# Optimization experiments

Hardware: AMD Instinct MI355X
Metric: run time of the kernel (lower is better)

The kernel has to match this reference:

```python
import jax, jax.numpy as jnp
import numpy as np

N_EP = 32          # episodes; 2*N_EP total sets (Dtrain + Dtest)
S = 1024           # points per set
IN_DIM = 255       # input feature dim
T_DIM = 1          # target dim
D = IN_DIM + T_DIM # attention-1 input dim = 256
L = 512            # latent_space_dim
K = 10             # n_discrete_states


def setup_inputs() -> dict:
    key = jax.random.key(0)
    ks = jax.random.split(key, 18)
    g = lambda k, sh, sc: (jax.random.normal(k, sh, dtype=jnp.float32) * sc)
    d = {
        "x_sets": g(ks[0], (2 * N_EP, S, IN_DIM), 1.0),
        "y_sets": g(ks[1], (2 * N_EP, S, T_DIM), 1.0),
        # self-attention layer 1 (D -> L), no pooling
        "Wq1": g(ks[2], (D, L), 1.0 / np.sqrt(D)), "bq1": jnp.zeros((L,), jnp.float32),
        "Wk1": g(ks[3], (D, L), 1.0 / np.sqrt(D)), "bk1": jnp.zeros((L,), jnp.float32),
        "Wv1": g(ks[4], (D, L), 1.0 / np.sqrt(D)), "bv1": jnp.zeros((L,), jnp.float32),
        # self-attention layer 2 (L -> L), mean pooling over set dim
        "Wq2": g(ks[5], (L, L), 1.0 / np.sqrt(L)), "bq2": jnp.zeros((L,), jnp.float32),
        "Wk2": g(ks[6], (L, L), 1.0 / np.sqrt(L)), "bk2": jnp.zeros((L,), jnp.float32),
        "Wv2": g(ks[7], (L, L), 1.0 / np.sqrt(L)), "bv2": jnp.zeros((L,), jnp.float32),
        # logit encoder Linear(L, L*K)
        "We": g(ks[8], (L, L * K), 1.0 / np.sqrt(L)),
        "be": jnp.zeros((L * K,), jnp.float32),
    }
    return d


def self_attention(x, Wq, bq, Wk, bk, Wv, bv, pool_mean):
    # x: [B, S, Din]; standard scaled dot-product self-attention
    q = x @ Wq + bq                                   # [B,S,L]
    k = x @ Wk + bk                                   # [B,S,L]
    v = x @ Wv + bv                                   # [B,S,L]
    scores = jnp.einsum('bqd,bkd->bqk', q, k) / jnp.sqrt(jnp.asarray(q.shape[-1], q.dtype))
    attn = jax.nn.softmax(scores, axis=-1)            # [B,S,S]
    out = jnp.einsum('bqk,bkd->bqd', attn, v)         # [B,S,L]
    if pool_mean:
        out = out.mean(axis=1)                        # [B,L]
    return out


def reference(x_sets, y_sets,
              Wq1, bq1, Wk1, bk1, Wv1, bv1,
              Wq2, bq2, Wk2, bk2, Wv2, bv2,
              We, be):
    # DatasetFeatureExtractor: cat(features, targets) -> attn -> relu -> attn(pool) -> relu
    x = jnp.concatenate([x_sets, y_sets], axis=-1)    # [2n,S,D]
    h = jax.nn.relu(self_attention(x, Wq1, bq1, Wk1, bk1, Wv1, bv1, pool_mean=False))
    phi = jax.nn.relu(self_attention(h, Wq2, bq2, Wk2, bk2, Wv2, bv2, pool_mean=True))  # [2n,L]
    # logit encode + log_softmax over discrete states
    logits = (phi @ We + be).reshape(-1, L, K)        # [2n,L,K]
    logp = jax.nn.log_softmax(logits, axis=2)
    log_probs_a, log_probs_b = logp[:N_EP], logp[N_EP:]
    return log_probs_a, log_probs_b
```

## Files before the change

kernel.cpp:

```cpp
#include <hip/hip_runtime.h>
#include <hip/hip_bf16.h>
#include <math.h>

#define NB      64
#define S_LEN   1024
#define IN_DIM  255
#define D_IN    256
#define L_DIM   512
#define K_CLS   10
#define QL_ELEMS (65536L * 512)

#define TILE 64
#define BKK  16

typedef __hip_bfloat16 bf16;
typedef __attribute__((ext_vector_type(8))) short short8;
typedef __attribute__((ext_vector_type(4))) float f32x4;

__device__ __forceinline__ float u2f(unsigned short u) {
    return __uint_as_float(((unsigned int)u) << 16);
}
__device__ __forceinline__ unsigned short f2bu(float x) {
    bf16 b = __float2bfloat16(x);
    return *reinterpret_cast<unsigned short*>(&b);
}

typedef const __attribute__((address_space(1))) unsigned int* gas_t;
typedef __attribute__((address_space(3))) unsigned int* las_t;
__device__ __forceinline__ void gload16(const bf16* g, bf16* l) {
    __builtin_amdgcn_global_load_lds((gas_t)(const void*)g, (las_t)(void*)l, 16, 0, 0);
}

__global__ __launch_bounds__(256) void build_xb(const float* __restrict__ xs,
                                                const float* __restrict__ ys,
                                                bf16* __restrict__ X) {
    long i = (long)blockIdx.x * 256 + threadIdx.x;
    long m = i >> 8;
    int  kk = (int)(i & 255);
    float v = (kk < IN_DIM) ? xs[m * IN_DIM + kk] : ys[m];
    X[i] = __float2bfloat16(v);
}

struct TW {
    const float* s0; const float* s1; const float* s2; const float* s3; const float* s4;
    bf16* d0; bf16* d1; bf16* d2; bf16* d3; bf16* d4;
    const float* bq1; const float* bk1; const float* bv1;
    const float* bq2; const float* bk2;
    float* biasQKV;
    float* bias2;
};
__global__ __launch_bounds__(256) void transpose_all(TW tw) {
    int i = blockIdx.x * 256 + threadIdx.x;
    if (i < 917504) {
        const float* S; bf16* D; int K, j;
        if (i < 131072)      { S = tw.s0; D = tw.d0; K = 256; j = i; }
        else if (i < 262144) { S = tw.s1; D = tw.d1; K = 256; j = i - 131072; }
        else if (i < 393216) { S = tw.s2; D = tw.d2; K = 256; j = i - 262144; }
        else if (i < 655360) { S = tw.s3; D = tw.d3; K = 512; j = i - 393216; }
        else                 { S = tw.s4; D = tw.d4; K = 512; j = i - 655360; }
        int n = j / K, k = j - n * K;
        D[j] = __float2bfloat16(S[(long)k * 512 + n]);
    } else if (i < 919040) {
        int j = i - 917504;
        float v = (j < 512) ? tw.bq1[j] : (j < 1024 ? tw.bk1[j - 512] : tw.bv1[j - 1024]);
        tw.biasQKV[j] = v;
    } else if (i < 920064) {
        int j = i - 919040;
        tw.bias2[j] = (j < 512) ? tw.bq2[j] : tw.bk2[j - 512];
    }
}

template <bool TRANSC, bool RELU, bool HASBIAS, bool EXPO, bool RSCALE, bool WRITEC, int FUSE, bool WCOL>
__global__ __launch_bounds__(256) void gemm_mfma(const bf16* __restrict__ A,
                                                 const bf16* __restrict__ B,
                                                 const float* __restrict__ bias,
                                                 bf16* __restrict__ C,
                                                 int K, long sA, long sB, long sC,
                                                 int ldc, float alpha,
                                                 float* __restrict__ ps,
                                                 const float* __restrict__ rsinv) {
    __shared__ bf16 As[2][128 * 32];
    __shared__ bf16 Bs[2][128 * 32];

    const int gx = gridDim.x, gy = gridDim.y;
    const int nwg = gx * gy * gridDim.z;
    int orig = blockIdx.x + gx * (blockIdx.y + gy * blockIdx.z);
    int id = ((nwg & 7) == 0) ? ((orig & 7) * (nwg >> 3) + (orig >> 3)) : orig;
    const int bx = id % gx;
    const int byz = id / gx;
    const int by = byz % gy;
    const int bz = byz / gy;

    A += (long)bz * sA;
    B += (long)bz * sB;
    C += (long)bz * sC;
    const int bm = by * 128;
    const int bn = bx * 128;
    const int t  = threadIdx.x;
    const int ln = t & 63;
    const int wv = t >> 6;
    const int wm = wv >> 1;
    const int wn = wv & 1;

    const bf16* gA = A + (long)(bm + (t >> 2)) * K + (t & 3) * 8;
    const bf16* gB = B + (long)(bn + (t >> 2)) * K + (t & 3) * 8;
    const int wb = wv * 512;

    f32x4 acc[4][4];
    #pragma unroll
    for (int i = 0; i < 4; ++i)
        #pragma unroll
        for (int j = 0; j < 4; ++j)
            #pragma unroll
            for (int q = 0; q < 4; ++q) acc[i][j][q] = 0.f;

    const int ro = ln & 15;
    const int ko = (ln >> 4) * 8;

    auto stage = [&](int buf, int k0) {
        gload16(gA + k0,          As[buf] + wb);
        gload16(gA + 64 * K + k0, As[buf] + wb + 2048);
        gload16(gB + k0,          Bs[buf] + wb);
        gload16(gB + 64 * K + k0, Bs[buf] + wb + 2048);
    };

    const int nt = K >> 5;
    stage(0, 0);
    __syncthreads();

    for (int tt = 0; tt < nt; ++tt) {
        const int cur = tt & 1;
        if (tt + 1 < nt) stage(cur ^ 1, (tt + 1) << 5);

        short8 af[4], bg[4];
        #pragma unroll
        for (int i = 0; i < 4; ++i) {
            af[i] = *(const short8*)(As[cur] + (wm * 64 + i * 16 + ro) * 32 + ko);
            bg[i] = *(const short8*)(Bs[cur] + (wn * 64 + i * 16 + ro) * 32 + ko);
        }
        #pragma unroll
        for (int i = 0; i < 4; ++i)
            #pragma unroll
            for (int j = 0; j < 4; ++j)
                acc[i][j] = __builtin_amdgcn_mfma_f32_16x16x32_bf16(af[i], bg[j], acc[i][j], 0, 0, 0);
        __syncthreads();
    }

    const int r0 = bm + wm * 64 + (ln >> 4) * 4;
    const int c0 = bn + wn * 64 + (ln & 15);

    if constexpr (FUSE > 0) {
        const int seg = bn >> 9;
        if (FUSE == 1 && seg == 2) {
            bf16* Cs = C + 2 * QL_ELEMS;
            #pragma unroll
            for (int i = 0; i < 4; ++i) {
                const int rowb = r0 + i * 16;
                #pragma unroll
                for (int j = 0; j < 4; ++j) {
                    const int col = c0 + j * 16;
                    const float bi = bias[col];
                    ushort4 o;
                    o.x = f2bu(acc[i][j][0] + bi);
                    o.y = f2bu(acc[i][j][1] + bi);
                    o.z = f2bu(acc[i][j][2] + bi);
                    o.w = f2bu(acc[i][j][3] + bi);
                    *(ushort4*)(Cs + (long)(col - 1024) * 1024 + rowb) = o;
                }
            }
        } else {
            bf16* Cs = C + (long)seg * QL_ELEMS;
            #pragma unroll
            for (int i = 0; i < 4; ++i) {
                #pragma unroll
                for (int j = 0; j < 4; ++j) {
                    const int col = c0 + j * 16;
                    const float bi = bias[col];
                    const int cl = col - seg * 512;
                    #pragma unroll
                    for (int q = 0; q < 4; ++q)
                        Cs[(long)(r0 + i * 16 + q) * 512 + cl] = __float2bfloat16(acc[i][j][q] + bi);
                }
            }
        }
    } else if constexpr (TRANSC) {
        #pragma unroll
        for (int i = 0; i < 4; ++i) {
            const int rowb = r0 + i * 16;
            #pragma unroll
            for (int j = 0; j < 4; ++j) {
                const int col = c0 + j * 16;
                const float bi = HASBIAS ? bias[col] : 0.f;
                ushort4 o;
                float v0 = acc[i][j][0] * alpha + bi;
                float v1 = acc[i][j][1] * alpha + bi;
                float v2 = acc[i][j][2] * alpha + bi;
                float v3 = acc[i][j][3] * alpha + bi;
                if (RELU) { v0 = fmaxf(v0, 0.f); v1 = fmaxf(v1, 0.f); v2 = fmaxf(v2, 0.f); v3 = fmaxf(v3, 0.f); }
                o.x = f2bu(v0); o.y = f2bu(v1); o.z = f2bu(v2); o.w = f2bu(v3);
                *(ushort4*)(C + (long)col * ldc + rowb) = o;
            }
        }
    } else if constexpr (EXPO) {
        float sloc[4][4];
        #pragma unroll
        for (int i = 0; i < 4; ++i)
            #pragma unroll
            for (int q = 0; q < 4; ++q) sloc[i][q] = 0.f;
        #pragma unroll
        for (int i = 0; i < 4; ++i) {
            #pragma unroll
            for (int j = 0; j < 4; ++j) {
                const int col = c0 + j * 16;
                #pragma unroll
                for (int q = 0; q < 4; ++q) {
                    float e = __expf(fminf(acc[i][j][q] * alpha, 80.f));
                    sloc[i][q] += e;
                    if (WRITEC) C[(long)(r0 + i * 16 + q) * ldc + col] = __float2bfloat16(e);
                }
            }
        }
        #pragma unroll
        for (int o = 1; o < 16; o <<= 1)
            #pragma unroll
            for (int i = 0; i < 4; ++i)
                #pragma unroll
                for (int q = 0; q < 4; ++q)
                    sloc[i][q] += __shfl_xor(sloc[i][q], o, 64);
        if ((ln & 15) == 0) {
            const int cb = bx * 2 + wn;
            const int rb = bm + wm * 64 + (ln >> 4) * 4;
            #pragma unroll
            for (int i = 0; i < 4; ++i)
                #pragma unroll
                for (int q = 0; q < 4; ++q)
                    ps[((long)bz * 16 + cb) * 1024 + rb + i * 16 + q] = sloc[i][q];
        }
    } else if constexpr (WCOL) {
        float rsv[4][4];
        const int rb = bm + wm * 64 + (ln >> 4) * 4;
        #pragma unroll
        for (int i = 0; i < 4; ++i)
            #pragma unroll
            for (int q = 0; q < 4; ++q)
                rsv[i][q] = rsinv[(long)bz * 1024 + rb + i * 16 + q];
        float cs[4];
        #pragma unroll
        for (int j = 0; j < 4; ++j) cs[j] = 0.f;
        #pragma unroll
        for (int i = 0; i < 4; ++i)
            #pragma unroll
            for (int j = 0; j < 4; ++j)
                #pragma unroll
                for (int q = 0; q < 4; ++q)
                    cs[j] += __expf(fminf(acc[i][j][q] * alpha, 80.f)) * rsv[i][q];
        #pragma unroll
        for (int j = 0; j < 4; ++j) {
            cs[j] += __shfl_xor(cs[j], 16, 64);
            cs[j] += __shfl_xor(cs[j], 32, 64);
        }
        if (ln < 16) {
            const int cb = by * 2 + wm;
            #pragma unroll
            for (int j = 0; j < 4; ++j)
                ps[((long)bz * 16 + cb) * 1024 + (bn + wn * 64 + j * 16 + ln)] = cs[j];
        }
    } else {
        float rsv[4][4];
        if constexpr (RSCALE) {
            const int rb = bm + wm * 64 + (ln >> 4) * 4;
            #pragma unroll
            for (int i = 0; i < 4; ++i)
                #pragma unroll
                for (int q = 0; q < 4; ++q)
                    rsv[i][q] = rsinv[(long)bz * 1024 + rb + i * 16 + q];
        }
        #pragma unroll
        for (int i = 0; i < 4; ++i) {
            #pragma unroll
            for (int j = 0; j < 4; ++j) {
                const int col = c0 + j * 16;
                const float bi = HASBIAS ? bias[col] : 0.f;
                #pragma unroll
                for (int q = 0; q < 4; ++q) {
                    float v = acc[i][j][q] * alpha + bi;
                    if (RSCALE) v *= rsv[i][q];
                    if (RELU) v = fmaxf(v, 0.f);
                    C[(long)(r0 + i * 16 + q) * ldc + col] = __float2bfloat16(v);
                }
            }
        }
    }
}

__global__ __launch_bounds__(256) void rowsum_inv(const float* __restrict__ ps,
                                                  float* __restrict__ rsinv, int n) {
    int i = blockIdx.x * 256 + threadIdx.x;
    if (i >= n) return;
    const int b = i >> 10, row = i & 1023;
    float s = 0.f;
    #pragma unroll
    for (int cb = 0; cb < 16; ++cb) s += ps[((long)b * 16 + cb) * 1024 + row];
    rsinv[i] = 1.f / s;
}

__global__ __launch_bounds__(256) void colsum_red(const float* __restrict__ wps,
                                                  float* __restrict__ w, int n) {
    int i = blockIdx.x * 256 + threadIdx.x;
    if (i >= n) return;
    const int b = i >> 10, col = i & 1023;
    float s = 0.f;
    #pragma unroll
    for (int cb = 0; cb < 16; ++cb) s += wps[((long)b * 16 + cb) * 1024 + col];
    w[i] = s;
}

template <bool RELU>
__global__ __launch_bounds__(256) void gemm_f32s(const float* __restrict__ A,
                                                 const float* __restrict__ B,
                                                 const float* __restrict__ bias,
                                                 float* __restrict__ C,
                                                 int M, int N, int K) {
    __shared__ float As[BKK][TILE + 1];
    __shared__ float Bs[BKK][TILE + 1];
    const int bm = blockIdx.y * TILE;
    const int bn = blockIdx.x * TILE;
    const int t  = threadIdx.x;
    const int tx = t & 15, ty = t >> 4;
    float acc[4][4] = {};
    for (int k0 = 0; k0 < K; k0 += BKK) {
        {
            int m  = t >> 2;
            int kq = (t & 3) * 4;
            const float4 av = *(const float4*)(A + (long)(bm + m) * K + k0 + kq);
            As[kq + 0][m] = av.x; As[kq + 1][m] = av.y;
            As[kq + 2][m] = av.z; As[kq + 3][m] = av.w;
        }
        {
            int k  = t >> 4;
            int nq = (t & 15) * 4;
            const float4 bv = *(const float4*)(B + (long)(k0 + k) * N + bn + nq);
            Bs[k][nq + 0] = bv.x; Bs[k][nq + 1] = bv.y;
            Bs[k][nq + 2] = bv.z; Bs[k][nq + 3] = bv.w;
        }
        __syncthreads();
        #pragma unroll
        for (int k = 0; k < BKK; ++k) {
            float a[4], bb[4];
            #pragma unroll
            for (int i = 0; i < 4; ++i) a[i] = As[k][ty * 4 + i];
            #pragma unroll
            for (int j = 0; j < 4; ++j) bb[j] = Bs[k][tx * 4 + j];
            #pragma unroll
            for (int i = 0; i < 4; ++i)
                #pragma unroll
                for (int j = 0; j < 4; ++j)
                    acc[i][j] = fmaf(a[i], bb[j], acc[i][j]);
        }
        __syncthreads();
    }
    #pragma unroll
    for (int i = 0; i < 4; ++i) {
        const int row  = bm + ty * 4 + i;
        const int col0 = bn + tx * 4;
        #pragma unroll
        for (int j = 0; j < 4; ++j) {
            float x = acc[i][j] + bias[col0 + j];
            if (RELU) x = fmaxf(x, 0.f);
            C[(long)row * N + col0 + j] = x;
        }
    }
}

__global__ __launch_bounds__(256) void pool_u_part(const bf16* __restrict__ h,
                                                   const float* __restrict__ w,
                                                   float* __restrict__ up) {
    const int b  = blockIdx.x;
    const int qq = blockIdx.y;
    const int t  = threadIdx.x;
    __shared__ float wl[256];
    wl[t] = w[b * S_LEN + qq * 256 + t];
    __syncthreads();
    const bf16* hp = h + (long)b * S_LEN * L_DIM + (long)qq * 256 * L_DIM;
    float a0 = 0.f, a1 = 0.f;
    for (int q = 0; q < 256; ++q) {
        ushort2 uv = *(const ushort2*)(hp + (long)q * L_DIM + t * 2);
        float ww = wl[q];
        a0 = fmaf(ww, u2f(uv.x), a0);
        a1 = fmaf(ww, u2f(uv.y), a1);
    }
    up[((long)(b * 4 + qq)) * L_DIM + t * 2 + 0] = a0;
    up[((long)(b * 4 + qq)) * L_DIM + t * 2 + 1] = a1;
}

__global__ __launch_bounds__(256) void pool_u_red(const float* __restrict__ up,
                                                  float* __restrict__ u) {
    int i = blockIdx.x * 256 + threadIdx.x;
    if (i >= NB * L_DIM) return;
    int b = i >> 9, d = i & 511;
    float s = up[((long)(b * 4 + 0)) * L_DIM + d] + up[((long)(b * 4 + 1)) * L_DIM + d]
            + up[((long)(b * 4 + 2)) * L_DIM + d] + up[((long)(b * 4 + 3)) * L_DIM + d];
    u[i] = s * (1.f / (float)S_LEN);
}

__global__ __launch_bounds__(256) void log_softmax10(const float* __restrict__ logits,
                                                     float* __restrict__ out) {
    const int t = blockIdx.x * 256 + threadIdx.x;
    if (t >= NB * L_DIM) return;
    const float* p = logits + (long)t * K_CLS;
    float v[K_CLS], m = -INFINITY;
    #pragma unroll
    for (int k = 0; k < K_CLS; ++k) { v[k] = p[k]; m = fmaxf(m, v[k]); }
    float s = 0.f;
    #pragma unroll
    for (int k = 0; k < K_CLS; ++k) s += __expf(v[k] - m);
    const float lse = m + logf(s);
    float* o = out + (long)t * K_CLS;
    #pragma unroll
    for (int k = 0; k < K_CLS; ++k) o[k] = v[k] - lse;
}

extern "C" void kernel_launch(void* const* d_in, const int* in_sizes, int n_in,
                              void* d_out, int out_size, void* d_ws, size_t ws_size,
                              hipStream_t stream) {
    const float* xs  = (const float*)d_in[0];
    const float* ys  = (const float*)d_in[1];
    const float* Wq1 = (const float*)d_in[2];  const float* bq1 = (const float*)d_in[3];
    const float* Wk1 = (const float*)d_in[4];  const float* bk1 = (const float*)d_in[5];
    const float* Wv1 = (const float*)d_in[6];  const float* bv1 = (const float*)d_in[7];
    const float* Wq2 = (const float*)d_in[8];  const float* bq2 = (const float*)d_in[9];
    const float* Wk2 = (const float*)d_in[10]; const float* bk2 = (const float*)d_in[11];
    const float* Wv2 = (const float*)d_in[12]; const float* bv2 = (const float*)d_in[13];
    const float* We  = (const float*)d_in[14]; const float* be  = (const float*)d_in[15];
    float* out = (float*)d_out;

    const long M  = (long)NB * S_LEN;
    const long QL = M * L_DIM;
    const long SL = (long)S_LEN * L_DIM;
    const long SS = (long)S_LEN * S_LEN;

    bf16* Xb  = (bf16*)d_ws;
    bf16* B1  = Xb + M * D_IN;
    bf16* B2  = B1 + QL;
    bf16* B3  = B2 + QL;
    bf16* WTb = B3 + QL;
    bf16* Wq1T = WTb;
    bf16* Wk1T = Wq1T + L_DIM * D_IN;
    bf16* Wv1T = Wk1T + L_DIM * D_IN;
    bf16* Wq2T = Wv1T + L_DIM * D_IN;
    bf16* Wk2T = Wq2T + L_DIM * L_DIM;
    bf16* Scb  = Wk2T + L_DIM * L_DIM;

    const size_t base_b = (size_t)((char*)Scb - (char*)d_ws);
    const size_t f32_b  = (size_t)(M + 2 * NB * L_DIM + NB * L_DIM * K_CLS
                                   + 64 * 16 * 1024 + 64 * 1024 + 4 * NB * L_DIM
                                   + 64 * 16 * 1024 + 1536 + 1024) * 4 + 256;
    int BCH1 = 16;
    while (BCH1 > 8 && base_b + (size_t)BCH1 * SS * 2 + f32_b > ws_size) BCH1 >>= 1;

    float* w       = (float*)(Scb + (long)BCH1 * SS);
    float* u       = w   + M / S_LEN * 1024;
    float* phi     = u   + NB * L_DIM;
    float* lg      = phi + NB * L_DIM;
    float* ps      = lg  + NB * L_DIM * K_CLS;
    float* rsinv   = ps  + 64 * 16 * 1024;
    float* up      = rsinv + 64 * 1024;
    float* wps     = up  + 4 * NB * L_DIM;
    float* biasQKV = wps + 64 * 16 * 1024;
    float* bias2   = biasQKV + 1536;

    const float inv_sqrt_L = 0.044194173824159216f;

    build_xb<<<dim3((unsigned)(M * D_IN / 256)), 256, 0, stream>>>(xs, ys, Xb);
    {
        TW tw { Wq1, Wk1, Wv1, Wq2, Wk2, Wq1T, Wk1T, Wv1T, Wq2T, Wk2T,
                bq1, bk1, bv1, bq2, bk2, biasQKV, bias2 };
        transpose_all<<<dim3(3595), 256, 0, stream>>>(tw);
    }

    {
        dim3 g(1536 / 128, S_LEN / 128, NB);
        gemm_mfma<false, false, true, false, false, true, 1, false><<<g, 256, 0, stream>>>(
            Xb, WTb, biasQKV, B1, D_IN, (long)S_LEN * D_IN, 0, SL, L_DIM, 1.f, nullptr, nullptr);
    }
    for (int c = 0; c < NB / BCH1; ++c) {
        const long aoff = (long)c * BCH1 * SL;
        float* psc = ps    + (long)c * BCH1 * 16 * 1024;
        float* rsc = rsinv + (long)c * BCH1 * 1024;
        dim3 gs(S_LEN / 128, S_LEN / 128, BCH1);
        gemm_mfma<false, false, false, true, false, true, 0, false><<<gs, 256, 0, stream>>>(
            B1 + aoff, B2 + aoff, nullptr, Scb, L_DIM, SL, SL, SS, S_LEN, inv_sqrt_L, psc, nullptr);
        rowsum_inv<<<dim3((unsigned)(BCH1 * S_LEN / 256)), 256, 0, stream>>>(psc, rsc, BCH1 * S_LEN);
        dim3 gp(L_DIM / 128, S_LEN / 128, BCH1);
        gemm_mfma<false, true, false, false, true, true, 0, false><<<gp, 256, 0, stream>>>(
            Scb, B3 + aoff, nullptr, B1 + aoff, S_LEN, SS, SL, SL, L_DIM, 1.f, nullptr, rsc);
    }
    {
        dim3 g(1024 / 128, S_LEN / 128, NB);
        gemm_mfma<false, false, true, false, false, true, 2, false><<<g, 256, 0, stream>>>(
            B1, Wq2T, bias2, B2, L_DIM, SL, 0, SL, L_DIM, 1.f, nullptr, nullptr);
    }
    {
        dim3 gs(S_LEN / 128, S_LEN / 128, NB);
        gemm_mfma<false, false, false, true, false, false, 0, false><<<gs, 256, 0, stream>>>(
            B2, B3, nullptr, Scb, L_DIM, SL, SL, 0, S_LEN, inv_sqrt_L, ps, nullptr);
        rowsum_inv<<<dim3((unsigned)(NB * S_LEN / 256)), 256, 0, stream>>>(ps, rsinv, NB * S_LEN);
        gemm_mfma<false, false, false, false, false, false, 0, true><<<gs, 256, 0, stream>>>(
            B2, B3, nullptr, Scb, L_DIM, SL, SL, 0, S_LEN, inv_sqrt_L, wps, rsinv);
        colsum_red<<<dim3((unsigned)(NB * S_LEN / 256)), 256, 0, stream>>>(wps, w, NB * S_LEN);
    }
    pool_u_part<<<dim3(NB, 4), 256, 0, stream>>>(B1, w, up);
    pool_u_red<<<dim3(NB * L_DIM / 256), 256, 0, stream>>>(up, u);
    gemm_f32s<true><<<dim3(L_DIM / TILE, 1), 256, 0, stream>>>(u, Wv2, bv2, phi, NB, L_DIM, L_DIM);
    gemm_f32s<false><<<dim3((L_DIM * K_CLS) / TILE, 1), 256, 0, stream>>>(phi, We, be, lg, NB, L_DIM * K_CLS, L_DIM);
    log_softmax10<<<dim3((NB * L_DIM + 255) / 256), 256, 0, stream>>>(lg, out);
}
```

Baseline: 831.9 us.

## Fold small reduction kernels into neighbouring GEMMs and merge prep launches

Merges build_xb into the weight-transpose prep kernel. The row-sum inverse is now computed inside the consuming GEMMs, which read the partial sums into shared memory. The column-sum reduction moves into pool_u_part, and the pool reduction plus mean scaling moves into the phi GEMM's A-tile load. This removes five small kernel launches and their intermediate buffers, and drops the unused TRANSC template path. In exchange, each GEMM block redundantly sums 16 partials per row, and pool blocks re-sum the column partials.

```diff
diff --git a/kernel.cpp b/kernel.cpp
--- a/kernel.cpp
+++ b/kernel.cpp
@@ -31,17 +31,8 @@
     __builtin_amdgcn_global_load_lds((gas_t)(const void*)g, (las_t)(void*)l, 16, 0, 0);
 }
 
-__global__ __launch_bounds__(256) void build_xb(const float* __restrict__ xs,
-                                                const float* __restrict__ ys,
-                                                bf16* __restrict__ X) {
-    long i = (long)blockIdx.x * 256 + threadIdx.x;
-    long m = i >> 8;
-    int  kk = (int)(i & 255);
-    float v = (kk < IN_DIM) ? xs[m * IN_DIM + kk] : ys[m];
-    X[i] = __float2bfloat16(v);
-}
-
 struct TW {
+    const float* xs; const float* ys; bf16* X;
     const float* s0; const float* s1; const float* s2; const float* s3; const float* s4;
     bf16* d0; bf16* d1; bf16* d2; bf16* d3; bf16* d4;
     const float* bq1; const float* bk1; const float* bv1;
@@ -49,28 +40,37 @@
     float* biasQKV;
     float* bias2;
 };
-__global__ __launch_bounds__(256) void transpose_all(TW tw) {
-    int i = blockIdx.x * 256 + threadIdx.x;
-    if (i < 917504) {
+#define X_ELEMS 16777216L
+__global__ __launch_bounds__(256) void prep_all(TW tw) {
+    long i = (long)blockIdx.x * 256 + threadIdx.x;
+    if (i < X_ELEMS) {
+        long m = i >> 8;
+        int  kk = (int)(i & 255);
+        float v = (kk < IN_DIM) ? tw.xs[m * IN_DIM + kk] : tw.ys[m];
+        tw.X[i] = __float2bfloat16(v);
+        return;
+    }
+    int j0 = (int)(i - X_ELEMS);
+    if (j0 < 917504) {
         const float* S; bf16* D; int K, j;
-        if (i < 131072)      { S = tw.s0; D = tw.d0; K = 256; j = i; }
-        else if (i < 262144) { S = tw.s1; D = tw.d1; K = 256; j = i - 131072; }
-        else if (i < 393216) { S = tw.s2; D = tw.d2; K = 256; j = i - 262144; }
-        else if (i < 655360) { S = tw.s3; D = tw.d3; K = 512; j = i - 393216; }
-        else                 { S = tw.s4; D = tw.d4; K = 512; j = i - 655360; }
+        if (j0 < 131072)      { S = tw.s0; D = tw.d0; K = 256; j = j0; }
+        else if (j0 < 262144) { S = tw.s1; D = tw.d1; K = 256; j = j0 - 131072; }
+        else if (j0 < 393216) { S = tw.s2; D = tw.d2; K = 256; j = j0 - 262144; }
+        else if (j0 < 655360) { S = tw.s3; D = tw.d3; K = 512; j = j0 - 393216; }
+        else                  { S = tw.s4; D = tw.d4; K = 512; j = j0 - 655360; }
         int n = j / K, k = j - n * K;
         D[j] = __float2bfloat16(S[(long)k * 512 + n]);
-    } else if (i < 919040) {
-        int j = i - 917504;
+    } else if (j0 < 919040) {
+        int j = j0 - 917504;
         float v = (j < 512) ? tw.bq1[j] : (j < 1024 ? tw.bk1[j - 512] : tw.bv1[j - 1024]);
         tw.biasQKV[j] = v;
-    } else if (i < 920064) {
-        int j = i - 919040;
+    } else if (j0 < 920064) {
+        int j = j0 - 919040;
         tw.bias2[j] = (j < 512) ? tw.bq2[j] : tw.bk2[j - 512];
     }
 }
 
-template <bool TRANSC, bool RELU, bool HASBIAS, bool EXPO, bool RSCALE, bool WRITEC, int FUSE, bool WCOL>
+template <bool RELU, bool HASBIAS, bool EXPO, bool RSCALE, bool WRITEC, int FUSE, bool WCOL>
 __global__ __launch_bounds__(256) void gemm_mfma(const bf16* __restrict__ A,
                                                  const bf16* __restrict__ B,
                                                  const float* __restrict__ bias,
@@ -78,9 +78,10 @@
                                                  int K, long sA, long sB, long sC,
                                                  int ldc, float alpha,
                                                  float* __restrict__ ps,
-                                                 const float* __restrict__ rsinv) {
+                                                 const float* __restrict__ psIn) {
     __shared__ bf16 As[2][128 * 32];
     __shared__ bf16 Bs[2][128 * 32];
+    __shared__ float rsl[128];
 
     const int gx = gridDim.x, gy = gridDim.y;
     const int nwg = gx * gy * gridDim.z;
@@ -105,6 +106,16 @@
     const bf16* gA = A + (long)(bm + (t >> 2)) * K + (t & 3) * 8;
     const bf16* gB = B + (long)(bn + (t >> 2)) * K + (t & 3) * 8;
     const int wb = wv * 512;
+
+    if constexpr (RSCALE || WCOL) {
+        if (t < 128) {
+            float s = 0.f;
+            #pragma unroll
+            for (int cb = 0; cb < 16; ++cb)
+                s += psIn[((long)bz * 16 + cb) * 1024 + bm + t];
+            rsl[t] = 1.f / s;
+        }
+    }
 
     f32x4 acc[4][4];
     #pragma unroll
@@ -183,24 +194,6 @@
                 }
             }
         }
-    } else if constexpr (TRANSC) {
-        #pragma unroll
-        for (int i = 0; i < 4; ++i) {
-            const int rowb = r0 + i * 16;
-            #pragma unroll
-            for (int j = 0; j < 4; ++j) {
-                const int col = c0 + j * 16;
-                const float bi = HASBIAS ? bias[col] : 0.f;
-                ushort4 o;
-                float v0 = acc[i][j][0] * alpha + bi;
-                float v1 = acc[i][j][1] * alpha + bi;
-                float v2 = acc[i][j][2] * alpha + bi;
-                float v3 = acc[i][j][3] * alpha + bi;
-                if (RELU) { v0 = fmaxf(v0, 0.f); v1 = fmaxf(v1, 0.f); v2 = fmaxf(v2, 0.f); v3 = fmaxf(v3, 0.f); }
-                o.x = f2bu(v0); o.y = f2bu(v1); o.z = f2bu(v2); o.w = f2bu(v3);
-                *(ushort4*)(C + (long)col * ldc + rowb) = o;
-            }
-        }
     } else if constexpr (EXPO) {
         float sloc[4][4];
         #pragma unroll
@@ -238,12 +231,12 @@
         }
     } else if constexpr (WCOL) {
         float rsv[4][4];
-        const int rb = bm + wm * 64 + (ln >> 4) * 4;
+        const int lr = wm * 64 + (ln >> 4) * 4;
         #pragma unroll
         for (int i = 0; i < 4; ++i)
             #pragma unroll
             for (int q = 0; q < 4; ++q)
-                rsv[i][q] = rsinv[(long)bz * 1024 + rb + i * 16 + q];
+                rsv[i][q] = rsl[lr + i * 16 + q];
         float cs[4];
         #pragma unroll
         for (int j = 0; j < 4; ++j) cs[j] = 0.f;
@@ -268,12 +261,12 @@
     } else {
         float rsv[4][4];
         if constexpr (RSCALE) {
-            const int rb = bm + wm * 64 + (ln >> 4) * 4;
+            const int lr = wm * 64 + (ln >> 4) * 4;
             #pragma unroll
             for (int i = 0; i < 4; ++i)
                 #pragma unroll
                 for (int q = 0; q < 4; ++q)
-                    rsv[i][q] = rsinv[(long)bz * 1024 + rb + i * 16 + q];
+                    rsv[i][q] = rsl[lr + i * 16 + q];
         }
         #pragma unroll
         for (int i = 0; i < 4; ++i) {
@@ -293,29 +286,93 @@
     }
 }
 
-__global__ __launch_bounds__(256) void rowsum_inv(const float* __restrict__ ps,
-                                                  float* __restrict__ rsinv, int n) {
-    int i = blockIdx.x * 256 + threadIdx.x;
-    if (i >= n) return;
-    const int b = i >> 10, row = i & 1023;
-    float s = 0.f;
+__global__ __launch_bounds__(256) void pool_u_part(const bf16* __restrict__ h,
+                                                   const float* __restrict__ wps,
+                                                   float* __restrict__ up) {
+    const int b  = blockIdx.x;
+    const int qq = blockIdx.y;
+    const int t  = threadIdx.x;
+    __shared__ float wl[256];
+    {
+        float s = 0.f;
+        #pragma unroll
+        for (int cb = 0; cb < 16; ++cb)
+            s += wps[((long)b * 16 + cb) * 1024 + qq * 256 + t];
+        wl[t] = s;
+    }
+    __syncthreads();
+    const bf16* hp = h + (long)b * S_LEN * L_DIM + (long)qq * 256 * L_DIM;
+    float a0 = 0.f, a1 = 0.f;
+    for (int q = 0; q < 256; ++q) {
+        ushort2 uv = *(const ushort2*)(hp + (long)q * L_DIM + t * 2);
+        float ww = wl[q];
+        a0 = fmaf(ww, u2f(uv.x), a0);
+        a1 = fmaf(ww, u2f(uv.y), a1);
+    }
+    up[((long)(b * 4 + qq)) * L_DIM + t * 2 + 0] = a0;
+    up[((long)(b * 4 + qq)) * L_DIM + t * 2 + 1] = a1;
+}
+
+__global__ __launch_bounds__(256) void gemm_phi(const float* __restrict__ up,
+                                                const float* __restrict__ B,
+                                                const float* __restrict__ bias,
+                                                float* __restrict__ C) {
+    __shared__ float As[BKK][TILE + 1];
+    __shared__ float Bs[BKK][TILE + 1];
+    const int bn = blockIdx.x * TILE;
+    const int t  = threadIdx.x;
+    const int tx = t & 15, ty = t >> 4;
+    float acc[4][4] = {};
+    for (int k0 = 0; k0 < L_DIM; k0 += BKK) {
+        {
+            int m  = t >> 2;
+            int kq = (t & 3) * 4;
+            const float* pb = up + (long)m * 4 * L_DIM + k0 + kq;
+            float4 p0 = *(const float4*)(pb);
+            float4 p1 = *(const float4*)(pb + L_DIM);
+            float4 p2 = *(const float4*)(pb + 2 * L_DIM);
+            float4 p3 = *(const float4*)(pb + 3 * L_DIM);
+            const float sc = 1.f / (float)S_LEN;
+            As[kq + 0][m] = (p0.x + p1.x + p2.x + p3.x) * sc;
+            As[kq + 1][m] = (p0.y + p1.y + p2.y + p3.y) * sc;
+            As[kq + 2][m] = (p0.z + p1.z + p2.z + p3.z) * sc;
+            As[kq + 3][m] = (p0.w + p1.w + p2.w + p3.w) * sc;
+        }
+        {
+            int k  = t >> 4;
+            int nq = (t & 15) * 4;
+            const float4 bv = *(const float4*)(B + (long)(k0 + k) * L_DIM + bn + nq);
+            Bs[k][nq + 0] = bv.x; Bs[k][nq + 1] = bv.y;
+            Bs[k][nq + 2] = bv.z; Bs[k][nq + 3] = bv.w;
+        }
+        __syncthreads();
+        #pragma unroll
+        for (int k = 0; k < BKK; ++k) {
+            float a[4], bb[4];
+            #pragma unroll
+            for (int i = 0; i < 4; ++i) a[i] = As[k][ty * 4 + i];
+            #pragma unroll
+            for (int j = 0; j < 4; ++j) bb[j] = Bs[k][tx * 4 + j];
+            #pragma unroll
+            for (int i = 0; i < 4; ++i)
+                #pragma unroll
+                for (int j = 0; j < 4; ++j)
+                    acc[i][j] = fmaf(a[i], bb[j], acc[i][j]);
+        }
+        __syncthreads();
+    }
     #pragma unroll
-    for (int cb = 0; cb < 16; ++cb) s += ps[((long)b * 16 + cb) * 1024 + row];
-    rsinv[i] = 1.f / s;
-}
-
-__global__ __launch_bounds__(256) void colsum_red(const float* __restrict__ wps,
-                                                  float* __restrict__ w, int n) {
-    int i = blockIdx.x * 256 + threadIdx.x;
-    if (i >= n) return;
-    const int b = i >> 10, col = i & 1023;
-    float s = 0.f;
-    #pragma unroll
-    for (int cb = 0; cb < 16; ++cb) s += wps[((long)b * 16 + cb) * 1024 + col];
-    w[i] = s;
-}
-
-template <bool RELU>
+    for (int i = 0; i < 4; ++i) {
+        const int row  = ty * 4 + i;
+        const int col0 = bn + tx * 4;
+        #pragma unroll
+        for (int j = 0; j < 4; ++j) {
+            float x = fmaxf(acc[i][j] + bias[col0 + j], 0.f);
+            C[(long)row * L_DIM + col0 + j] = x;
+        }
+    }
+}
+
 __global__ __launch_bounds__(256) void gemm_f32s(const float* __restrict__ A,
                                                  const float* __restrict__ B,
                                                  const float* __restrict__ bias,
@@ -365,42 +422,9 @@
         const int col0 = bn + tx * 4;
         #pragma unroll
         for (int j = 0; j < 4; ++j) {
-            float x = acc[i][j] + bias[col0 + j];
-            if (RELU) x = fmaxf(x, 0.f);
-            C[(long)row * N + col0 + j] = x;
-        }
-    }
-}
-
-__global__ __launch_bounds__(256) void pool_u_part(const bf16* __restrict__ h,
-                                                   const float* __restrict__ w,
-                                                   float* __restrict__ up) {
-    const int b  = blockIdx.x;
-    const int qq = blockIdx.y;
-    const int t  = threadIdx.x;
-    __shared__ float wl[256];
-    wl[t] = w[b * S_LEN + qq * 256 + t];
-    __syncthreads();
-    const bf16* hp = h + (long)b * S_LEN * L_DIM + (long)qq * 256 * L_DIM;
-    float a0 = 0.f, a1 = 0.f;
-    for (int q = 0; q < 256; ++q) {
-        ushort2 uv = *(const ushort2*)(hp + (long)q * L_DIM + t * 2);
-        float ww = wl[q];
-        a0 = fmaf(ww, u2f(uv.x), a0);
-        a1 = fmaf(ww, u2f(uv.y), a1);
-    }
-    up[((long)(b * 4 + qq)) * L_DIM + t * 2 + 0] = a0;
-    up[((long)(b * 4 + qq)) * L_DIM + t * 2 + 1] = a1;
-}
-
-__global__ __launch_bounds__(256) void pool_u_red(const float* __restrict__ up,
-                                                  float* __restrict__ u) {
-    int i = blockIdx.x * 256 + threadIdx.x;
-    if (i >= NB * L_DIM) return;
-    int b = i >> 9, d = i & 511;
-    float s = up[((long)(b * 4 + 0)) * L_DIM + d] + up[((long)(b * 4 + 1)) * L_DIM + d]
-            + up[((long)(b * 4 + 2)) * L_DIM + d] + up[((long)(b * 4 + 3)) * L_DIM + d];
-    u[i] = s * (1.f / (float)S_LEN);
+            C[(long)row * N + col0 + j] = acc[i][j] + bias[col0 + j];
+        }
+    }
 }
 
 __global__ __launch_bounds__(256) void log_softmax10(const float* __restrict__ logits,
@@ -452,66 +476,57 @@
     bf16* Scb  = Wk2T + L_DIM * L_DIM;
 
     const size_t base_b = (size_t)((char*)Scb - (char*)d_ws);
-    const size_t f32_b  = (size_t)(M + 2 * NB * L_DIM + NB * L_DIM * K_CLS
-                                   + 64 * 16 * 1024 + 64 * 1024 + 4 * NB * L_DIM
+    const size_t f32_b  = (size_t)(NB * L_DIM + NB * L_DIM * K_CLS
+                                   + 64 * 16 * 1024 + 4 * NB * L_DIM
                                    + 64 * 16 * 1024 + 1536 + 1024) * 4 + 256;
     int BCH1 = 16;
     while (BCH1 > 8 && base_b + (size_t)BCH1 * SS * 2 + f32_b > ws_size) BCH1 >>= 1;
 
-    float* w       = (float*)(Scb + (long)BCH1 * SS);
-    float* u       = w   + M / S_LEN * 1024;
-    float* phi     = u   + NB * L_DIM;
+    float* phi     = (float*)(Scb + (long)BCH1 * SS);
     float* lg      = phi + NB * L_DIM;
     float* ps      = lg  + NB * L_DIM * K_CLS;
-    float* rsinv   = ps  + 64 * 16 * 1024;
-    float* up      = rsinv + 64 * 1024;
+    float* up      = ps  + 64 * 16 * 1024;
     float* wps     = up  + 4 * NB * L_DIM;
     float* biasQKV = wps + 64 * 16 * 1024;
     float* bias2   = biasQKV + 1536;
 
     const float inv_sqrt_L = 0.044194173824159216f;
 
-    build_xb<<<dim3((unsigned)(M * D_IN / 256)), 256, 0, stream>>>(xs, ys, Xb);
     {
-        TW tw { Wq1, Wk1, Wv1, Wq2, Wk2, Wq1T, Wk1T, Wv1T, Wq2T, Wk2T,
+        TW tw { xs, ys, Xb, Wq1, Wk1, Wv1, Wq2, Wk2, Wq1T, Wk1T, Wv1T, Wq2T, Wk2T,
                 bq1, bk1, bv1, bq2, bk2, biasQKV, bias2 };
-        transpose_all<<<dim3(3595), 256, 0, stream>>>(tw);
+        prep_all<<<dim3((unsigned)((X_ELEMS + 920064 + 255) / 256)), 256, 0, stream>>>(tw);
     }
 
     {
         dim3 g(1536 / 128, S_LEN / 128, NB);
-        gemm_mfma<false, false, true, false, false, true, 1, false><<<g, 256, 0, stream>>>(
+        gemm_mfma<false, true, false, false, true, 1, false><<<g, 256, 0, stream>>>(
             Xb, WTb, biasQKV, B1, D_IN, (long)S_LEN * D_IN, 0, SL, L_DIM, 1.f, nullptr, nullptr);
     }
     for (int c = 0; c < NB / BCH1; ++c) {
         const long aoff = (long)c * BCH1 * SL;
-        float* psc = ps    + (long)c * BCH1 * 16 * 1024;
-        float* rsc = rsinv + (long)c * BCH1 * 1024;
+        float* psc = ps + (long)c * BCH1 * 16 * 1024;
         dim3 gs(S_LEN / 128, S_LEN / 128, BCH1);
-        gemm_mfma<false, false, false, true, false, true, 0, false><<<gs, 256, 0, stream>>>(
+        gemm_mfma<false, false, true, false, true, 0, false><<<gs, 256, 0, stream>>>(
             B1 + aoff, B2 + aoff, nullptr, Scb, L_DIM, SL, SL, SS, S_LEN, inv_sqrt_L, psc, nullptr);
-        rowsum_inv<<<dim3((unsigned)(BCH1 * S_LEN / 256)), 256, 0, stream>>>(psc, rsc, BCH1 * S_LEN);
         dim3 gp(L_DIM / 128, S_LEN / 128, BCH1);
-        gemm_mfma<false, true, false, false, true, true, 0, false><<<gp, 256, 0, stream>>>(
-            Scb, B3 + aoff, nullptr, B1 + aoff, S_LEN, SS, SL, SL, L_DIM, 1.f, nullptr, rsc);
+        gemm_mfma<true, false, false, true, true, 0, false><<<gp, 256, 0, stream>>>(
+            Scb, B3 + aoff, nullptr, B1 + aoff, S_LEN, SS, SL, SL, L_DIM, 1.f, nullptr, psc);
     }
     {
         dim3 g(1024 / 128, S_LEN / 128, NB);
-        gemm_mfma<false, false, true, false, false, true, 2, false><<<g, 256, 0, stream>>>(
+        gemm_mfma<false, true, false, false, true, 2, false><<<g, 256, 0, stream>>>(
             B1, Wq2T, bias2, B2, L_DIM, SL, 0, SL, L_DIM, 1.f, nullptr, nullptr);
     }
     {
         dim3 gs(S_LEN / 128, S_LEN / 128, NB);
-        gemm_mfma<false, false, false, true, false, false, 0, false><<<gs, 256, 0, stream>>>(
+        gemm_mfma<false, false, true, false, false, 0, false><<<gs, 256, 0, stream>>>(
             B2, B3, nullptr, Scb, L_DIM, SL, SL, 0, S_LEN, inv_sqrt_L, ps, nullptr);
-        rowsum_inv<<<dim3((unsigned)(NB * S_LEN / 256)), 256, 0, stream>>>(ps, rsinv, NB * S_LEN);
-        gemm_mfma<false, false, false, false, false, false, 0, true><<<gs, 256, 0, stream>>>(
-            B2, B3, nullptr, Scb, L_DIM, SL, SL, 0, S_LEN, inv_sqrt_L, wps, rsinv);
-        colsum_red<<<dim3((unsigned)(NB * S_LEN / 256)), 256, 0, stream>>>(wps, w, NB * S_LEN);
-    }
-    pool_u_part<<<dim3(NB, 4), 256, 0, stream>>>(B1, w, up);
-    pool_u_red<<<dim3(NB * L_DIM / 256), 256, 0, stream>>>(up, u);
-    gemm_f32s<true><<<dim3(L_DIM / TILE, 1), 256, 0, stream>>>(u, Wv2, bv2, phi, NB, L_DIM, L_DIM);
-    gemm_f32s<false><<<dim3((L_DIM * K_CLS) / TILE, 1), 256, 0, stream>>>(phi, We, be, lg, NB, L_DIM * K_CLS, L_DIM);
+        gemm_mfma<false, false, false, false, false, 0, true><<<gs, 256, 0, stream>>>(
+            B2, B3, nullptr, Scb, L_DIM, SL, SL, 0, S_LEN, inv_sqrt_L, wps, ps);
+    }
+    pool_u_part<<<dim3(NB, 4), 256, 0, stream>>>(B1, wps, up);
+    gemm_phi<<<dim3(L_DIM / TILE, 1), 256, 0, stream>>>(up, Wv2, bv2, phi);
+    gemm_f32s<<<dim3((L_DIM * K_CLS) / TILE, 1), 256, 0, stream>>>(phi, We, be, lg, NB, L_DIM * K_CLS, L_DIM);
     log_softmax10<<<dim3((NB * L_DIM + 255) / 256), 256, 0, stream>>>(lg, out);
 }
```

Measured after the change: 804.4 us. 1.03x faster.
